# Kernel tuning notes

Hardware: AMD Instinct MI355X
Metric: run time of the kernel (lower is better)

## Reference

```python
import jax, jax.numpy as jnp
import numpy as np

N_NODES = 50000
N_EDGES = 300000
IN_FEATS = 128
N_HIDDEN = 64
N_HEADS = 4
N_CLASSES = 47
NEG_SLOPE = 0.2


def setup_inputs() -> dict:
    key = jax.random.key(0)
    ks = jax.random.split(key, 16)
    s = 0.1
    inp = {
        "x": jax.random.normal(ks[0], (N_NODES, IN_FEATS), jnp.float32),
        "src": jax.random.randint(ks[1], (N_EDGES,), 0, N_NODES, jnp.int64 if jax.config.jax_enable_x64 else jnp.int32),
        "dst": jax.random.randint(ks[2], (N_EDGES,), 0, N_NODES, jnp.int64 if jax.config.jax_enable_x64 else jnp.int32),
        # layer 1: in_feats -> (heads, hidden)
        "W1": jax.random.normal(ks[3], (IN_FEATS, N_HEADS * N_HIDDEN), jnp.float32) * s,
        "al1": jax.random.normal(ks[4], (N_HEADS, N_HIDDEN), jnp.float32) * s,
        "ar1": jax.random.normal(ks[5], (N_HEADS, N_HIDDEN), jnp.float32) * s,
        "b1": jnp.zeros((N_HEADS * N_HIDDEN,), jnp.float32),
        # layer 2: heads*hidden -> (heads, hidden)
        "W2": jax.random.normal(ks[6], (N_HEADS * N_HIDDEN, N_HEADS * N_HIDDEN), jnp.float32) * s,
        "al2": jax.random.normal(ks[7], (N_HEADS, N_HIDDEN), jnp.float32) * s,
        "ar2": jax.random.normal(ks[8], (N_HEADS, N_HIDDEN), jnp.float32) * s,
        "b2": jnp.zeros((N_HEADS * N_HIDDEN,), jnp.float32),
        # layer 3: heads*hidden -> (1, n_classes)
        "W3": jax.random.normal(ks[9], (N_HEADS * N_HIDDEN, N_CLASSES), jnp.float32) * s,
        "al3": jax.random.normal(ks[10], (1, N_CLASSES), jnp.float32) * s,
        "ar3": jax.random.normal(ks[11], (1, N_CLASSES), jnp.float32) * s,
        "b3": jnp.zeros((N_CLASSES,), jnp.float32),
    }
    return inp


def gat_conv(h, src, dst, W, al, ar, b, n_nodes):
    """DGL GATConv (shared src/dst projection, edge-softmax over dst)."""
    H, D = al.shape
    feat = (h @ W).reshape(n_nodes, H, D)              # [N,H,D]
    el = jnp.sum(feat * al[None], axis=-1)             # [N,H]
    er = jnp.sum(feat * ar[None], axis=-1)             # [N,H]
    e = jax.nn.leaky_relu(el[src] + er[dst], NEG_SLOPE)  # [E,H]
    emax = jax.ops.segment_max(e, dst, num_segments=n_nodes)  # [N,H]
    emax = jnp.where(jnp.isfinite(emax), emax, 0.0)    # empty segments
    ee = jnp.exp(e - emax[dst])                        # [E,H]
    denom = jax.ops.segment_sum(ee, dst, num_segments=n_nodes)  # [N,H]
    alpha = ee / jnp.maximum(denom[dst], 1e-9)         # [E,H]
    msg = feat[src] * alpha[..., None]                 # [E,H,D]
    out = jax.ops.segment_sum(msg, dst, num_segments=n_nodes)   # [N,H,D]
    return out + b.reshape(1, H, D)


def reference(x, src, dst, W1, al1, ar1, b1, W2, al2, ar2, b2, W3, al3, ar3, b3):
    n = x.shape[0]
    h = gat_conv(x, src, dst, W1, al1, ar1, b1, n).reshape(n, -1)  # flatten heads
    h = gat_conv(h, src, dst, W2, al2, ar2, b2, n).reshape(n, -1)
    h = gat_conv(h, src, dst, W3, al3, ar3, b3, n)                 # [N,1,C]
    return h.mean(axis=1)                                          # [N,C]
```

## Files before the change

kernel.cpp:

```cpp
#include <hip/hip_runtime.h>
#include <cstddef>

#define GAT_N 50000
#define GAT_E 300000
#define SCAN_B 256

typedef short bf16x8 __attribute__((ext_vector_type(8)));
typedef float f32x4  __attribute__((ext_vector_type(4)));
typedef unsigned int u32;

__device__ __forceinline__ ushort f2bf(float f) {
    unsigned u = __float_as_uint(f);
    return (ushort)((u + 0x7fffu + ((u >> 16) & 1u)) >> 16);
}
__device__ __forceinline__ float bf2f(ushort h) {
    return __uint_as_float((unsigned)h << 16);
}

__device__ __forceinline__ void gload16(const ushort* g, ushort* l) {
    __builtin_amdgcn_global_load_lds(
        (const __attribute__((address_space(1))) u32*)g,
        (__attribute__((address_space(3))) u32*)l, 16, 0, 0);
}


__global__ __launch_bounds__(256) void zero_ints(int* __restrict__ a, int n) {
    int i = blockIdx.x * blockDim.x + threadIdx.x;
    int stride = gridDim.x * blockDim.x;
    for (; i < n; i += stride) a[i] = 0;
}

__global__ __launch_bounds__(256) void count_k(
    const int* __restrict__ dst, int* __restrict__ cnt, int E)
{
    int e = blockIdx.x * blockDim.x + threadIdx.x;
    if (e < E) atomicAdd(&cnt[dst[e]], 1);
}

__global__ __launch_bounds__(256) void csr_partial(
    const int* __restrict__ cnt, int* __restrict__ partials, int N, int chunk)
{
    __shared__ int red[256];
    int b = blockIdx.x, t = threadIdx.x;
    int s = 0;
    for (int i = t; i < chunk; i += 256) {
        int idx = b * chunk + i;
        if (idx < N) s += cnt[idx];
    }
    red[t] = s;
    __syncthreads();
    for (int off = 128; off > 0; off >>= 1) {
        if (t < off) red[t] += red[t + off];
        __syncthreads();
    }
    if (t == 0) partials[b] = red[0];
}

__global__ __launch_bounds__(SCAN_B) void csr_scanp(
    int* __restrict__ partials, int* __restrict__ rowptr, int N)
{
    __shared__ int sc[SCAN_B];
    int t = threadIdx.x;
    int v = partials[t];
    sc[t] = v;
    __syncthreads();
    for (int off = 1; off < SCAN_B; off <<= 1) {
        int u = (t >= off) ? sc[t - off] : 0;
        __syncthreads();
        sc[t] += u;
        __syncthreads();
    }
    partials[t] = sc[t] - v;
    if (t == SCAN_B - 1) rowptr[N] = sc[t];
}

__global__ __launch_bounds__(256) void csr_write(
    const int* __restrict__ cnt, const int* __restrict__ partials,
    int* __restrict__ rowptr, int N, int chunk)
{
    __shared__ int sc[256];
    int b = blockIdx.x, t = threadIdx.x;
    int idx = b * chunk + t;
    int v = (t < chunk && idx < N) ? cnt[idx] : 0;
    sc[t] = v;
    __syncthreads();
    for (int off = 1; off < 256; off <<= 1) {
        int u = (t >= off) ? sc[t - off] : 0;
        __syncthreads();
        sc[t] += u;
        __syncthreads();
    }
    if (t < chunk && idx < N) rowptr[idx] = partials[b] + sc[t] - v;
}

__global__ __launch_bounds__(256) void scatter_k(
    const int* __restrict__ src, const int* __restrict__ dst,
    const int* __restrict__ rowptr, int* __restrict__ cursor,
    int* __restrict__ ssrc, int* __restrict__ sdst, int E)
{
    int e = blockIdx.x * blockDim.x + threadIdx.x;
    if (e >= E) return;
    int d = dst[e];
    int p = rowptr[d] + atomicAdd(&cursor[d], 1);
    ssrc[p] = src[e];
    sdst[p] = d;
}


__global__ __launch_bounds__(256) void convert_x(
    const float* __restrict__ x, ushort* __restrict__ Xh, ushort* __restrict__ Xl,
    long total4)
{
    long i = (long)blockIdx.x * blockDim.x + threadIdx.x;
    long stride = (long)gridDim.x * blockDim.x;
    for (; i < total4; i += stride) {
        float4 v = *(const float4*)(x + i * 4);
        ushort4 h, lo;
        h.x = f2bf(v.x); lo.x = f2bf(v.x - bf2f(h.x));
        h.y = f2bf(v.y); lo.y = f2bf(v.y - bf2f(h.y));
        h.z = f2bf(v.z); lo.z = f2bf(v.z - bf2f(h.z));
        h.w = f2bf(v.w); lo.w = f2bf(v.w - bf2f(h.w));
        *(ushort4*)(Xh + i * 4) = h;
        *(ushort4*)(Xl + i * 4) = lo;
    }
}

__global__ __launch_bounds__(256) void convert_w(
    const float* __restrict__ W, ushort* __restrict__ Wth, ushort* __restrict__ Wtl,
    int K, int M, int Mp)
{
    int idx = blockIdx.x * blockDim.x + threadIdx.x;
    if (idx >= Mp * K) return;
    int c = idx / K, k = idx - c * K;
    float v = (c < M) ? W[(size_t)k * M + c] : 0.f;
    ushort h = f2bf(v);
    Wth[idx] = h;
    Wtl[idx] = f2bf(v - bf2f(h));
}


__global__ __launch_bounds__(256) void gemm_feat(
    const ushort* __restrict__ Ah, const ushort* __restrict__ Al,
    const ushort* __restrict__ Wh, const ushort* __restrict__ Wl,
    const float* __restrict__ alw, const float* __restrict__ arw,
    float* __restrict__ feat, float* __restrict__ el, float* __restrict__ er,
    int N, int K, int M, int H, int D, int ldF)
{
    __shared__ ushort lds[2 * 12288];

    const int m0 = blockIdx.x * 64;
    const int n0 = blockIdx.y * 128;
    const int t = threadIdx.x;
    const int w = t >> 6, lane = t & 63;
    const int lr = lane & 15, lg = lane >> 4;
    const int wr = (w >> 1) * 32, wc = (w & 1) * 64;
    const int NK = K >> 5;

    const ushort* srcp[6];
    u32 lbase[6];
    #pragma unroll
    for (int l = 0; l < 6; ++l) {
        int ub = l * 256 + w * 64;
        int u = ub + lane;
        const ushort* s;
        if (u < 512) {
            int half = u >> 8;
            int v = u & 255;
            int rowblk = v >> 6, kc = (v >> 4) & 3, r = v & 15;
            int grow = m0 + rowblk * 16 + r;
            grow = grow < N ? grow : N - 1;
            s = (half ? Al : Ah) + (size_t)grow * K + kc * 8;
        } else {
            int v = u - 512;
            int half = v >> 9;
            int b = v & 511;
            int cb = b >> 6, kc = (b >> 4) & 3, c = b & 15;
            int gcol = n0 + cb * 16 + c;
            s = (half ? Wl : Wh) + (size_t)gcol * K + kc * 8;
        }
        srcp[l] = s;
        lbase[l] = (u32)(ub * 8);
    }

    f32x4 acc[2][4] = {};

    #pragma unroll
    for (int l = 0; l < 6; ++l) {
        gload16(srcp[l], &lds[lbase[l]]);
        srcp[l] += 32;
    }
    __syncthreads();

    int cur = 0;
    for (int kt = 0; kt < NK; ++kt) {
        if (kt + 1 < NK) {
            int nb = (cur ^ 1) * 12288;
            #pragma unroll
            for (int l = 0; l < 6; ++l) {
                gload16(srcp[l], &lds[nb + lbase[l]]);
                srcp[l] += 32;
            }
        }
        const ushort* buf = lds + cur * 12288;
        const int rb = (w >> 1) * 2;
        const int cbb = (w & 1) * 4;
        bf16x8 a_h[2], a_l[2];
        #pragma unroll
        for (int fi = 0; fi < 2; ++fi) {
            int idx = ((rb + fi) * 4 + lg) * 128 + lr * 8;
            a_h[fi] = *(const bf16x8*)&buf[idx];
            a_l[fi] = *(const bf16x8*)&buf[2048 + idx];
        }
        #pragma unroll
        for (int fj = 0; fj < 4; ++fj) {
            int idx = ((cbb + fj) * 4 + lg) * 128 + lr * 8;
            bf16x8 b_h = *(const bf16x8*)&buf[4096 + idx];
            bf16x8 b_l = *(const bf16x8*)&buf[8192 + idx];
            #pragma unroll
            for (int fi = 0; fi < 2; ++fi) {
                acc[fi][fj] = __builtin_amdgcn_mfma_f32_16x16x32_bf16(a_h[fi], b_h, acc[fi][fj], 0, 0, 0);
                acc[fi][fj] = __builtin_amdgcn_mfma_f32_16x16x32_bf16(a_l[fi], b_h, acc[fi][fj], 0, 0, 0);
                acc[fi][fj] = __builtin_amdgcn_mfma_f32_16x16x32_bf16(a_h[fi], b_l, acc[fi][fj], 0, 0, 0);
            }
        }
        __syncthreads();
        cur ^= 1;
    }

    #pragma unroll
    for (int fi = 0; fi < 2; ++fi) {
        #pragma unroll
        for (int q = 0; q < 4; ++q) {
            int row = m0 + wr + fi * 16 + 4 * lg + q;
            if (row < N) {
                #pragma unroll
                for (int fj = 0; fj < 4; ++fj) {
                    int col = n0 + wc + fj * 16 + lr;
                    if (col < M) feat[(size_t)row * ldF + col] = acc[fi][fj][q];
                }
            }
        }
    }

    const int head = (n0 + wc) / D;
    if (head < H) {
        float alv[4], arv[4];
        #pragma unroll
        for (int fj = 0; fj < 4; ++fj) {
            int col = n0 + wc + fj * 16 + lr;
            alv[fj] = (col < M) ? alw[col] : 0.f;
            arv[fj] = (col < M) ? arw[col] : 0.f;
        }
        #pragma unroll
        for (int fi = 0; fi < 2; ++fi) {
            #pragma unroll
            for (int q = 0; q < 4; ++q) {
                float s1 = 0.f, s2 = 0.f;
                #pragma unroll
                for (int fj = 0; fj < 4; ++fj) {
                    s1 = fmaf(acc[fi][fj][q], alv[fj], s1);
                    s2 = fmaf(acc[fi][fj][q], arv[fj], s2);
                }
                #pragma unroll
                for (int mask = 1; mask <= 8; mask <<= 1) {
                    s1 += __shfl_xor(s1, mask);
                    s2 += __shfl_xor(s2, mask);
                }
                int row = m0 + wr + fi * 16 + 4 * lg + q;
                if (lr == 0 && row < N) {
                    el[(size_t)row * H + head] = s1;
                    er[(size_t)row * H + head] = s2;
                }
            }
        }
    }
}


__global__ __launch_bounds__(256) void edge_score4(
    const int* __restrict__ ssrc, const int* __restrict__ sdst,
    const float* __restrict__ el, const float* __restrict__ er,
    float* __restrict__ sc, int E)
{
    int p = blockIdx.x * blockDim.x + threadIdx.x;
    if (p >= E) return;
    int s = ssrc[p], d = sdst[p];
    float4 a = *(const float4*)(el + (size_t)s * 4);
    float4 b = *(const float4*)(er + (size_t)d * 4);
    float4 v;
    v.x = a.x + b.x; v.x = v.x > 0.f ? v.x : 0.2f * v.x;
    v.y = a.y + b.y; v.y = v.y > 0.f ? v.y : 0.2f * v.y;
    v.z = a.z + b.z; v.z = v.z > 0.f ? v.z : 0.2f * v.z;
    v.w = a.w + b.w; v.w = v.w > 0.f ? v.w : 0.2f * v.w;
    *(float4*)(sc + (size_t)p * 4) = v;
}

__global__ __launch_bounds__(256) void edge_score1(
    const int* __restrict__ ssrc, const int* __restrict__ sdst,
    const float* __restrict__ el, const float* __restrict__ er,
    float* __restrict__ sc, int E)
{
    int p = blockIdx.x * blockDim.x + threadIdx.x;
    if (p >= E) return;
    float v = el[ssrc[p]] + er[sdst[p]];
    sc[p] = v > 0.f ? v : 0.2f * v;
}


__global__ __launch_bounds__(256) void node_aggr256(
    const int* __restrict__ rowptr, const int* __restrict__ ssrc,
    const float* __restrict__ sc, const float* __restrict__ feat,
    const float* __restrict__ bias,
    ushort* __restrict__ Ah_out, ushort* __restrict__ Al_out, int N)
{
    int n = blockIdx.x * 4 + (threadIdx.x >> 6);
    if (n >= N) return;
    int lane = threadIdx.x & 63;
    int h = lane >> 4, sub = lane & 15;
    int beg = rowptr[n], end = rowptr[n + 1];

    float m = -__builtin_inff();
    for (int j = beg + sub; j < end; j += 16)
        m = fmaxf(m, sc[(size_t)j * 4 + h]);
    #pragma unroll
    for (int mask = 1; mask <= 8; mask <<= 1)
        m = fmaxf(m, __shfl_xor(m, mask));

    float denom = 0.f;
    for (int j = beg + sub; j < end; j += 16)
        denom += __expf(sc[(size_t)j * 4 + h] - m);
    #pragma unroll
    for (int mask = 1; mask <= 8; mask <<= 1)
        denom += __shfl_xor(denom, mask);

    float inv = 1.f / fmaxf(denom, 1e-9f);
    float ax = 0.f, ay = 0.f, az = 0.f, aw = 0.f;
    int j = beg;
    for (; j + 4 <= end; j += 4) {
        int s0 = ssrc[j + 0], s1 = ssrc[j + 1], s2 = ssrc[j + 2], s3 = ssrc[j + 3];
        float w0 = __expf(sc[(size_t)(j + 0) * 4 + h] - m);
        float w1 = __expf(sc[(size_t)(j + 1) * 4 + h] - m);
        float w2 = __expf(sc[(size_t)(j + 2) * 4 + h] - m);
        float w3 = __expf(sc[(size_t)(j + 3) * 4 + h] - m);
        float4 f0 = *(const float4*)(feat + (size_t)s0 * 256 + lane * 4);
        float4 f1 = *(const float4*)(feat + (size_t)s1 * 256 + lane * 4);
        float4 f2 = *(const float4*)(feat + (size_t)s2 * 256 + lane * 4);
        float4 f3 = *(const float4*)(feat + (size_t)s3 * 256 + lane * 4);
        ax = fmaf(w0, f0.x, fmaf(w1, f1.x, fmaf(w2, f2.x, fmaf(w3, f3.x, ax))));
        ay = fmaf(w0, f0.y, fmaf(w1, f1.y, fmaf(w2, f2.y, fmaf(w3, f3.y, ay))));
        az = fmaf(w0, f0.z, fmaf(w1, f1.z, fmaf(w2, f2.z, fmaf(w3, f3.z, az))));
        aw = fmaf(w0, f0.w, fmaf(w1, f1.w, fmaf(w2, f2.w, fmaf(w3, f3.w, aw))));
    }
    for (; j < end; ++j) {
        float wgt = __expf(sc[(size_t)j * 4 + h] - m);
        int s = ssrc[j];
        float4 f = *(const float4*)(feat + (size_t)s * 256 + lane * 4);
        ax = fmaf(wgt, f.x, ax);
        ay = fmaf(wgt, f.y, ay);
        az = fmaf(wgt, f.z, az);
        aw = fmaf(wgt, f.w, aw);
    }
    float v0 = fmaf(ax, inv, bias[lane * 4 + 0]);
    float v1 = fmaf(ay, inv, bias[lane * 4 + 1]);
    float v2 = fmaf(az, inv, bias[lane * 4 + 2]);
    float v3 = fmaf(aw, inv, bias[lane * 4 + 3]);
    ushort4 hh, lo;
    hh.x = f2bf(v0); lo.x = f2bf(v0 - bf2f(hh.x));
    hh.y = f2bf(v1); lo.y = f2bf(v1 - bf2f(hh.y));
    hh.z = f2bf(v2); lo.z = f2bf(v2 - bf2f(hh.z));
    hh.w = f2bf(v3); lo.w = f2bf(v3 - bf2f(hh.w));
    *(ushort4*)(Ah_out + (size_t)n * 256 + lane * 4) = hh;
    *(ushort4*)(Al_out + (size_t)n * 256 + lane * 4) = lo;
}

__global__ __launch_bounds__(256) void node_aggr47(
    const int* __restrict__ rowptr, const int* __restrict__ ssrc,
    const float* __restrict__ sc, const float* __restrict__ feat,
    const float* __restrict__ bias, float* __restrict__ out, int N)
{
    int n = blockIdx.x * 4 + (threadIdx.x >> 6);
    if (n >= N) return;
    int lane = threadIdx.x & 63;
    int beg = rowptr[n], end = rowptr[n + 1];

    float m = -__builtin_inff();
    for (int j = beg + lane; j < end; j += 64)
        m = fmaxf(m, sc[j]);
    #pragma unroll
    for (int mask = 1; mask <= 32; mask <<= 1)
        m = fmaxf(m, __shfl_xor(m, mask));

    float denom = 0.f;
    for (int j = beg + lane; j < end; j += 64)
        denom += __expf(sc[j] - m);
    #pragma unroll
    for (int mask = 1; mask <= 32; mask <<= 1)
        denom += __shfl_xor(denom, mask);

    float inv = 1.f / fmaxf(denom, 1e-9f);
    float acc = 0.f;
    int j = beg;
    for (; j + 4 <= end; j += 4) {
        int s0 = ssrc[j + 0], s1 = ssrc[j + 1], s2 = ssrc[j + 2], s3 = ssrc[j + 3];
        float w0 = __expf(sc[j + 0] - m);
        float w1 = __expf(sc[j + 1] - m);
        float w2 = __expf(sc[j + 2] - m);
        float w3 = __expf(sc[j + 3] - m);
        float f0 = (lane < 47) ? feat[(size_t)s0 * 48 + lane] : 0.f;
        float f1 = (lane < 47) ? feat[(size_t)s1 * 48 + lane] : 0.f;
        float f2 = (lane < 47) ? feat[(size_t)s2 * 48 + lane] : 0.f;
        float f3 = (lane < 47) ? feat[(size_t)s3 * 48 + lane] : 0.f;
        acc = fmaf(w0, f0, fmaf(w1, f1, fmaf(w2, f2, fmaf(w3, f3, acc))));
    }
    for (; j < end; ++j) {
        float wgt = __expf(sc[j] - m);
        int s = ssrc[j];
        float f = (lane < 47) ? feat[(size_t)s * 48 + lane] : 0.f;
        acc = fmaf(wgt, f, acc);
    }
    if (lane < 47)
        out[(size_t)n * 47 + lane] = fmaf(acc, inv, bias[lane]);
}


extern "C" void kernel_launch(void* const* d_in, const int* in_sizes, int n_in,
                              void* d_out, int out_size, void* d_ws, size_t ws_size,
                              hipStream_t stream) {
    const float* x   = (const float*)d_in[0];
    const int*   src = (const int*)d_in[1];
    const int*   dst = (const int*)d_in[2];
    const float* W1  = (const float*)d_in[3];
    const float* al1 = (const float*)d_in[4];
    const float* ar1 = (const float*)d_in[5];
    const float* b1  = (const float*)d_in[6];
    const float* W2  = (const float*)d_in[7];
    const float* al2 = (const float*)d_in[8];
    const float* ar2 = (const float*)d_in[9];
    const float* b2  = (const float*)d_in[10];
    const float* W3  = (const float*)d_in[11];
    const float* al3 = (const float*)d_in[12];
    const float* ar3 = (const float*)d_in[13];
    const float* b3  = (const float*)d_in[14];
    float* out = (float*)d_out;

    const int N = GAT_N, E = GAT_E;
    const int chunk = (N + SCAN_B - 1) / SCAN_B;

    char* wsb = (char*)d_ws;
    size_t o = 0;
    float*  feat  = (float*)(wsb + o);  o += (size_t)N * 256 * 4;
    ushort* Ah    = (ushort*)(wsb + o); o += (size_t)N * 256 * 2;
    ushort* Al    = (ushort*)(wsb + o); o += (size_t)N * 256 * 2;
    float*  el    = (float*)(wsb + o);  o += (size_t)N * 4 * 4;
    float*  er    = (float*)(wsb + o);  o += (size_t)N * 4 * 4;
    int* rowptr   = (int*)(wsb + o);    o += (size_t)(N + 1) * 4;
    int* cnt      = (int*)(wsb + o);    o += (size_t)N * 4;
    int* cursor   = (int*)(wsb + o);    o += (size_t)N * 4;
    int* ssrc     = (int*)(wsb + o);    o += (size_t)E * 4;
    int* sdst     = (int*)(wsb + o);    o += (size_t)E * 4;
    float* scbuf  = (float*)(wsb + o);  o += (size_t)E * 4 * 4;
    int* partials = (int*)(wsb + o);    o += (size_t)SCAN_B * 4;
    ushort* Wt1h  = (ushort*)(wsb + o); o += (size_t)256 * 128 * 2;
    ushort* Wt1l  = (ushort*)(wsb + o); o += (size_t)256 * 128 * 2;
    ushort* Wt2h  = (ushort*)(wsb + o); o += (size_t)256 * 256 * 2;
    ushort* Wt2l  = (ushort*)(wsb + o); o += (size_t)256 * 256 * 2;
    ushort* Wt3h  = (ushort*)(wsb + o); o += (size_t)128 * 256 * 2;
    ushort* Wt3l  = (ushort*)(wsb + o); o += (size_t)128 * 256 * 2;
    ushort* Xh = Ah;
    ushort* Xl = Al;

    dim3 blk(256);
    int gE = (E + 255) / 256;
    int gN = (N + 3) / 4;
    dim3 gemmG((N + 63) / 64, 2);
    dim3 gemmG3((N + 63) / 64, 1);

    zero_ints<<<64, blk, 0, stream>>>(cnt, 2 * N);
    count_k<<<gE, blk, 0, stream>>>(dst, cnt, E);
    csr_partial<<<SCAN_B, blk, 0, stream>>>(cnt, partials, N, chunk);
    csr_scanp<<<1, SCAN_B, 0, stream>>>(partials, rowptr, N);
    csr_write<<<SCAN_B, blk, 0, stream>>>(cnt, partials, rowptr, N, chunk);
    scatter_k<<<gE, blk, 0, stream>>>(src, dst, rowptr, cursor, ssrc, sdst, E);

    convert_x<<<2048, blk, 0, stream>>>(x, Xh, Xl, (long)N * 128 / 4);
    convert_w<<<(256 * 128 + 255) / 256, blk, 0, stream>>>(W1, Wt1h, Wt1l, 128, 256, 256);
    convert_w<<<(256 * 256 + 255) / 256, blk, 0, stream>>>(W2, Wt2h, Wt2l, 256, 256, 256);
    convert_w<<<(128 * 256 + 255) / 256, blk, 0, stream>>>(W3, Wt3h, Wt3l, 256, 47, 128);

    gemm_feat<<<gemmG, blk, 0, stream>>>(Xh, Xl, Wt1h, Wt1l, al1, ar1,
                                         feat, el, er, N, 128, 256, 4, 64, 256);
    edge_score4<<<gE, blk, 0, stream>>>(ssrc, sdst, el, er, scbuf, E);
    node_aggr256<<<gN, blk, 0, stream>>>(rowptr, ssrc, scbuf, feat, b1, Ah, Al, N);

    gemm_feat<<<gemmG, blk, 0, stream>>>(Ah, Al, Wt2h, Wt2l, al2, ar2,
                                         feat, el, er, N, 256, 256, 4, 64, 256);
    edge_score4<<<gE, blk, 0, stream>>>(ssrc, sdst, el, er, scbuf, E);
    node_aggr256<<<gN, blk, 0, stream>>>(rowptr, ssrc, scbuf, feat, b2, Ah, Al, N);

    gemm_feat<<<gemmG3, blk, 0, stream>>>(Ah, Al, Wt3h, Wt3l, al3, ar3,
                                          feat, el, er, N, 256, 47, 1, 47, 48);
    edge_score1<<<gE, blk, 0, stream>>>(ssrc, sdst, el, er, scbuf, E);
    node_aggr47<<<gN, blk, 0, stream>>>(rowptr, ssrc, scbuf, feat, b3, out, N);
}
```

Before: 325.3 us.

## Enlarge GEMM row tile to 128 and process two nodes per wavefront in aggregation

The feature GEMM tile grows from 64 to 128 rows per block, so each wave computes a 4x4 grid of MFMA fragments and the weight tiles loaded into LDS are reused across twice as many rows. The 256-wide aggregation kernel now handles two destination nodes per wavefront and interleaves their gathers, aiming to keep more independent feature loads in flight. In exchange, GEMM blocks use more LDS and accumulator registers, which can lower occupancy. The aggregation does masked dummy loads whenever the two nodes have unequal degree.

```diff
diff --git a/kernel.cpp b/kernel.cpp
--- a/kernel.cpp
+++ b/kernel.cpp
@@ -146,46 +146,43 @@
     float* __restrict__ feat, float* __restrict__ el, float* __restrict__ er,
     int N, int K, int M, int H, int D, int ldF)
 {
-    __shared__ ushort lds[2 * 12288];
-
-    const int m0 = blockIdx.x * 64;
+    __shared__ ushort lds[2 * 16384];
+
+    const int m0 = blockIdx.x * 128;
     const int n0 = blockIdx.y * 128;
     const int t = threadIdx.x;
     const int w = t >> 6, lane = t & 63;
     const int lr = lane & 15, lg = lane >> 4;
-    const int wr = (w >> 1) * 32, wc = (w & 1) * 64;
+    const int wrb = (w >> 1) * 4;
+    const int wcb = (w & 1) * 4;
     const int NK = K >> 5;
 
-    const ushort* srcp[6];
-    u32 lbase[6];
-    #pragma unroll
-    for (int l = 0; l < 6; ++l) {
+    const ushort* srcp[8];
+    u32 lbase[8];
+    #pragma unroll
+    for (int l = 0; l < 8; ++l) {
         int ub = l * 256 + w * 64;
         int u = ub + lane;
+        int region = u >> 9;
+        int v = u & 511;
+        int rowblk = v >> 6, kc = (v >> 4) & 3, rc = v & 15;
         const ushort* s;
-        if (u < 512) {
-            int half = u >> 8;
-            int v = u & 255;
-            int rowblk = v >> 6, kc = (v >> 4) & 3, r = v & 15;
-            int grow = m0 + rowblk * 16 + r;
+        if (region < 2) {
+            int grow = m0 + rowblk * 16 + rc;
             grow = grow < N ? grow : N - 1;
-            s = (half ? Al : Ah) + (size_t)grow * K + kc * 8;
+            s = (region ? Al : Ah) + (size_t)grow * K + kc * 8;
         } else {
-            int v = u - 512;
-            int half = v >> 9;
-            int b = v & 511;
-            int cb = b >> 6, kc = (b >> 4) & 3, c = b & 15;
-            int gcol = n0 + cb * 16 + c;
-            s = (half ? Wl : Wh) + (size_t)gcol * K + kc * 8;
+            int gcol = n0 + rowblk * 16 + rc;
+            s = ((region & 1) ? Wl : Wh) + (size_t)gcol * K + kc * 8;
         }
         srcp[l] = s;
         lbase[l] = (u32)(ub * 8);
     }
 
-    f32x4 acc[2][4] = {};
-
-    #pragma unroll
-    for (int l = 0; l < 6; ++l) {
+    f32x4 acc[4][4] = {};
+
+    #pragma unroll
+    for (int l = 0; l < 8; ++l) {
         gload16(srcp[l], &lds[lbase[l]]);
         srcp[l] += 32;
     }
@@ -194,30 +191,28 @@
     int cur = 0;
     for (int kt = 0; kt < NK; ++kt) {
         if (kt + 1 < NK) {
-            int nb = (cur ^ 1) * 12288;
+            int nb = (cur ^ 1) * 16384;
             #pragma unroll
-            for (int l = 0; l < 6; ++l) {
+            for (int l = 0; l < 8; ++l) {
                 gload16(srcp[l], &lds[nb + lbase[l]]);
                 srcp[l] += 32;
             }
         }
-        const ushort* buf = lds + cur * 12288;
-        const int rb = (w >> 1) * 2;
-        const int cbb = (w & 1) * 4;
-        bf16x8 a_h[2], a_l[2];
+        const ushort* buf = lds + cur * 16384;
+        bf16x8 a_h[4], a_l[4];
         #pragma unroll
-        for (int fi = 0; fi < 2; ++fi) {
-            int idx = ((rb + fi) * 4 + lg) * 128 + lr * 8;
-            a_h[fi] = *(const bf16x8*)&buf[idx];
-            a_l[fi] = *(const bf16x8*)&buf[2048 + idx];
+        for (int fi = 0; fi < 4; ++fi) {
+            int aidx = ((wrb + fi) * 4 + lg) * 128 + lr * 8;
+            a_h[fi] = *(const bf16x8*)&buf[aidx];
+            a_l[fi] = *(const bf16x8*)&buf[4096 + aidx];
         }
         #pragma unroll
         for (int fj = 0; fj < 4; ++fj) {
-            int idx = ((cbb + fj) * 4 + lg) * 128 + lr * 8;
-            bf16x8 b_h = *(const bf16x8*)&buf[4096 + idx];
-            bf16x8 b_l = *(const bf16x8*)&buf[8192 + idx];
+            int bidx = ((wcb + fj) * 4 + lg) * 128 + lr * 8;
+            bf16x8 b_h = *(const bf16x8*)&buf[8192 + bidx];
+            bf16x8 b_l = *(const bf16x8*)&buf[12288 + bidx];
             #pragma unroll
-            for (int fi = 0; fi < 2; ++fi) {
+            for (int fi = 0; fi < 4; ++fi) {
                 acc[fi][fj] = __builtin_amdgcn_mfma_f32_16x16x32_bf16(a_h[fi], b_h, acc[fi][fj], 0, 0, 0);
                 acc[fi][fj] = __builtin_amdgcn_mfma_f32_16x16x32_bf16(a_l[fi], b_h, acc[fi][fj], 0, 0, 0);
                 acc[fi][fj] = __builtin_amdgcn_mfma_f32_16x16x32_bf16(a_h[fi], b_l, acc[fi][fj], 0, 0, 0);
@@ -228,31 +223,31 @@
     }
 
     #pragma unroll
-    for (int fi = 0; fi < 2; ++fi) {
+    for (int fi = 0; fi < 4; ++fi) {
         #pragma unroll
         for (int q = 0; q < 4; ++q) {
-            int row = m0 + wr + fi * 16 + 4 * lg + q;
+            int row = m0 + (w >> 1) * 64 + fi * 16 + 4 * lg + q;
             if (row < N) {
                 #pragma unroll
                 for (int fj = 0; fj < 4; ++fj) {
-                    int col = n0 + wc + fj * 16 + lr;
+                    int col = n0 + (w & 1) * 64 + fj * 16 + lr;
                     if (col < M) feat[(size_t)row * ldF + col] = acc[fi][fj][q];
                 }
             }
         }
     }
 
-    const int head = (n0 + wc) / D;
+    const int head = (n0 + (w & 1) * 64) / D;
     if (head < H) {
         float alv[4], arv[4];
         #pragma unroll
         for (int fj = 0; fj < 4; ++fj) {
-            int col = n0 + wc + fj * 16 + lr;
+            int col = n0 + (w & 1) * 64 + fj * 16 + lr;
             alv[fj] = (col < M) ? alw[col] : 0.f;
             arv[fj] = (col < M) ? arw[col] : 0.f;
         }
         #pragma unroll
-        for (int fi = 0; fi < 2; ++fi) {
+        for (int fi = 0; fi < 4; ++fi) {
             #pragma unroll
             for (int q = 0; q < 4; ++q) {
                 float s1 = 0.f, s2 = 0.f;
@@ -266,7 +261,7 @@
                     s1 += __shfl_xor(s1, mask);
                     s2 += __shfl_xor(s2, mask);
                 }
-                int row = m0 + wr + fi * 16 + 4 * lg + q;
+                int row = m0 + (w >> 1) * 64 + fi * 16 + 4 * lg + q;
                 if (lr == 0 && row < N) {
                     el[(size_t)row * H + head] = s1;
                     er[(size_t)row * H + head] = s2;
@@ -313,64 +308,92 @@
     const float* __restrict__ bias,
     ushort* __restrict__ Ah_out, ushort* __restrict__ Al_out, int N)
 {
-    int n = blockIdx.x * 4 + (threadIdx.x >> 6);
-    if (n >= N) return;
+    int wid = blockIdx.x * 4 + (threadIdx.x >> 6);
+    int na = wid * 2;
+    if (na >= N) return;
+    int nb = na + 1;
+    bool hb = nb < N;
     int lane = threadIdx.x & 63;
     int h = lane >> 4, sub = lane & 15;
-    int beg = rowptr[n], end = rowptr[n + 1];
-
-    float m = -__builtin_inff();
-    for (int j = beg + sub; j < end; j += 16)
-        m = fmaxf(m, sc[(size_t)j * 4 + h]);
-    #pragma unroll
-    for (int mask = 1; mask <= 8; mask <<= 1)
-        m = fmaxf(m, __shfl_xor(m, mask));
-
-    float denom = 0.f;
-    for (int j = beg + sub; j < end; j += 16)
-        denom += __expf(sc[(size_t)j * 4 + h] - m);
-    #pragma unroll
-    for (int mask = 1; mask <= 8; mask <<= 1)
-        denom += __shfl_xor(denom, mask);
-
-    float inv = 1.f / fmaxf(denom, 1e-9f);
-    float ax = 0.f, ay = 0.f, az = 0.f, aw = 0.f;
-    int j = beg;
-    for (; j + 4 <= end; j += 4) {
-        int s0 = ssrc[j + 0], s1 = ssrc[j + 1], s2 = ssrc[j + 2], s3 = ssrc[j + 3];
-        float w0 = __expf(sc[(size_t)(j + 0) * 4 + h] - m);
-        float w1 = __expf(sc[(size_t)(j + 1) * 4 + h] - m);
-        float w2 = __expf(sc[(size_t)(j + 2) * 4 + h] - m);
-        float w3 = __expf(sc[(size_t)(j + 3) * 4 + h] - m);
+    int begA = rowptr[na], endA = rowptr[na + 1];
+    int begB = 0, endB = 0;
+    if (hb) { begB = rowptr[nb]; endB = rowptr[nb + 1]; }
+
+    float ma = -__builtin_inff(), mb = -__builtin_inff();
+    for (int j = begA + sub; j < endA; j += 16) ma = fmaxf(ma, sc[(size_t)j * 4 + h]);
+    for (int j = begB + sub; j < endB; j += 16) mb = fmaxf(mb, sc[(size_t)j * 4 + h]);
+    #pragma unroll
+    for (int mask = 1; mask <= 8; mask <<= 1) {
+        ma = fmaxf(ma, __shfl_xor(ma, mask));
+        mb = fmaxf(mb, __shfl_xor(mb, mask));
+    }
+
+    float dena = 0.f, denb = 0.f;
+    for (int j = begA + sub; j < endA; j += 16) dena += __expf(sc[(size_t)j * 4 + h] - ma);
+    for (int j = begB + sub; j < endB; j += 16) denb += __expf(sc[(size_t)j * 4 + h] - mb);
+    #pragma unroll
+    for (int mask = 1; mask <= 8; mask <<= 1) {
+        dena += __shfl_xor(dena, mask);
+        denb += __shfl_xor(denb, mask);
+    }
+    float invA = 1.f / fmaxf(dena, 1e-9f);
+    float invB = 1.f / fmaxf(denb, 1e-9f);
+
+    int degA = endA - begA, degB = endB - begB;
+    int dmax = degA > degB ? degA : degB;
+
+    float a0 = 0.f, a1 = 0.f, a2 = 0.f, a3 = 0.f;
+    float b0 = 0.f, b1 = 0.f, b2 = 0.f, b3 = 0.f;
+    for (int k = 0; k < dmax; k += 2) {
+        bool v0 = k < degA,     v1 = k + 1 < degA;
+        bool v2 = k < degB,     v3 = k + 1 < degB;
+        int i0 = v0 ? begA + k     : 0;
+        int i1 = v1 ? begA + k + 1 : 0;
+        int i2 = v2 ? begB + k     : 0;
+        int i3 = v3 ? begB + k + 1 : 0;
+        int s0 = ssrc[i0], s1 = ssrc[i1], s2 = ssrc[i2], s3 = ssrc[i3];
+        float w0 = v0 ? __expf(sc[(size_t)i0 * 4 + h] - ma) : 0.f;
+        float w1 = v1 ? __expf(sc[(size_t)i1 * 4 + h] - ma) : 0.f;
+        float w2 = v2 ? __expf(sc[(size_t)i2 * 4 + h] - mb) : 0.f;
+        float w3 = v3 ? __expf(sc[(size_t)i3 * 4 + h] - mb) : 0.f;
         float4 f0 = *(const float4*)(feat + (size_t)s0 * 256 + lane * 4);
         float4 f1 = *(const float4*)(feat + (size_t)s1 * 256 + lane * 4);
         float4 f2 = *(const float4*)(feat + (size_t)s2 * 256 + lane * 4);
         float4 f3 = *(const float4*)(feat + (size_t)s3 * 256 + lane * 4);
-        ax = fmaf(w0, f0.x, fmaf(w1, f1.x, fmaf(w2, f2.x, fmaf(w3, f3.x, ax))));
-        ay = fmaf(w0, f0.y, fmaf(w1, f1.y, fmaf(w2, f2.y, fmaf(w3, f3.y, ay))));
-        az = fmaf(w0, f0.z, fmaf(w1, f1.z, fmaf(w2, f2.z, fmaf(w3, f3.z, az))));
-        aw = fmaf(w0, f0.w, fmaf(w1, f1.w, fmaf(w2, f2.w, fmaf(w3, f3.w, aw))));
-    }
-    for (; j < end; ++j) {
-        float wgt = __expf(sc[(size_t)j * 4 + h] - m);
-        int s = ssrc[j];
-        float4 f = *(const float4*)(feat + (size_t)s * 256 + lane * 4);
-        ax = fmaf(wgt, f.x, ax);
-        ay = fmaf(wgt, f.y, ay);
-        az = fmaf(wgt, f.z, az);
-        aw = fmaf(wgt, f.w, aw);
-    }
-    float v0 = fmaf(ax, inv, bias[lane * 4 + 0]);
-    float v1 = fmaf(ay, inv, bias[lane * 4 + 1]);
-    float v2 = fmaf(az, inv, bias[lane * 4 + 2]);
-    float v3 = fmaf(aw, inv, bias[lane * 4 + 3]);
-    ushort4 hh, lo;
-    hh.x = f2bf(v0); lo.x = f2bf(v0 - bf2f(hh.x));
-    hh.y = f2bf(v1); lo.y = f2bf(v1 - bf2f(hh.y));
-    hh.z = f2bf(v2); lo.z = f2bf(v2 - bf2f(hh.z));
-    hh.w = f2bf(v3); lo.w = f2bf(v3 - bf2f(hh.w));
-    *(ushort4*)(Ah_out + (size_t)n * 256 + lane * 4) = hh;
-    *(ushort4*)(Al_out + (size_t)n * 256 + lane * 4) = lo;
+        a0 = fmaf(w0, f0.x, fmaf(w1, f1.x, a0));
+        a1 = fmaf(w0, f0.y, fmaf(w1, f1.y, a1));
+        a2 = fmaf(w0, f0.z, fmaf(w1, f1.z, a2));
+        a3 = fmaf(w0, f0.w, fmaf(w1, f1.w, a3));
+        b0 = fmaf(w2, f2.x, fmaf(w3, f3.x, b0));
+        b1 = fmaf(w2, f2.y, fmaf(w3, f3.y, b1));
+        b2 = fmaf(w2, f2.z, fmaf(w3, f3.z, b2));
+        b3 = fmaf(w2, f2.w, fmaf(w3, f3.w, b3));
+    }
+
+    float bs0 = bias[lane * 4 + 0], bs1 = bias[lane * 4 + 1];
+    float bs2 = bias[lane * 4 + 2], bs3 = bias[lane * 4 + 3];
+    {
+        float v0 = fmaf(a0, invA, bs0), v1 = fmaf(a1, invA, bs1);
+        float v2 = fmaf(a2, invA, bs2), v3 = fmaf(a3, invA, bs3);
+        ushort4 hh, lo;
+        hh.x = f2bf(v0); lo.x = f2bf(v0 - bf2f(hh.x));
+        hh.y = f2bf(v1); lo.y = f2bf(v1 - bf2f(hh.y));
+        hh.z = f2bf(v2); lo.z = f2bf(v2 - bf2f(hh.z));
+        hh.w = f2bf(v3); lo.w = f2bf(v3 - bf2f(hh.w));
+        *(ushort4*)(Ah_out + (size_t)na * 256 + lane * 4) = hh;
+        *(ushort4*)(Al_out + (size_t)na * 256 + lane * 4) = lo;
+    }
+    if (hb) {
+        float v0 = fmaf(b0, invB, bs0), v1 = fmaf(b1, invB, bs1);
+        float v2 = fmaf(b2, invB, bs2), v3 = fmaf(b3, invB, bs3);
+        ushort4 hh, lo;
+        hh.x = f2bf(v0); lo.x = f2bf(v0 - bf2f(hh.x));
+        hh.y = f2bf(v1); lo.y = f2bf(v1 - bf2f(hh.y));
+        hh.z = f2bf(v2); lo.z = f2bf(v2 - bf2f(hh.z));
+        hh.w = f2bf(v3); lo.w = f2bf(v3 - bf2f(hh.w));
+        *(ushort4*)(Ah_out + (size_t)nb * 256 + lane * 4) = hh;
+        *(ushort4*)(Al_out + (size_t)nb * 256 + lane * 4) = lo;
+    }
 }
 
 __global__ __launch_bounds__(256) void node_aggr47(
@@ -472,8 +495,9 @@
     dim3 blk(256);
     int gE = (E + 255) / 256;
     int gN = (N + 3) / 4;
-    dim3 gemmG((N + 63) / 64, 2);
-    dim3 gemmG3((N + 63) / 64, 1);
+    int gN2 = ((N + 1) / 2 + 3) / 4;
+    dim3 gemmG((N + 127) / 128, 2);
+    dim3 gemmG3((N + 127) / 128, 1);
 
     zero_ints<<<64, blk, 0, stream>>>(cnt, 2 * N);
     count_k<<<gE, blk, 0, stream>>>(dst, cnt, E);
@@ -490,12 +514,12 @@
     gemm_feat<<<gemmG, blk, 0, stream>>>(Xh, Xl, Wt1h, Wt1l, al1, ar1,
                                          feat, el, er, N, 128, 256, 4, 64, 256);
     edge_score4<<<gE, blk, 0, stream>>>(ssrc, sdst, el, er, scbuf, E);
-    node_aggr256<<<gN, blk, 0, stream>>>(rowptr, ssrc, scbuf, feat, b1, Ah, Al, N);
+    node_aggr256<<<gN2, blk, 0, stream>>>(rowptr, ssrc, scbuf, feat, b1, Ah, Al, N);
 
     gemm_feat<<<gemmG, blk, 0, stream>>>(Ah, Al, Wt2h, Wt2l, al2, ar2,
                                          feat, el, er, N, 256, 256, 4, 64, 256);
     edge_score4<<<gE, blk, 0, stream>>>(ssrc, sdst, el, er, scbuf, E);
-    node_aggr256<<<gN, blk, 0, stream>>>(rowptr, ssrc, scbuf, feat, b2, Ah, Al, N);
+    node_aggr256<<<gN2, blk, 0, stream>>>(rowptr, ssrc, scbuf, feat, b2, Ah, Al, N);
 
     gemm_feat<<<gemmG3, blk, 0, stream>>>(Ah, Al, Wt3h, Wt3l, al3, ar3,
                                           feat, el, er, N, 256, 47, 1, 47, 48);
```

Result: no change. 326.5 us (+0.4%).
